# Kernel optimization log

Hardware: AMD Instinct MI355X
Metric: run time of the kernel (lower is better)

Reference implementation:

```python
import jax, jax.numpy as jnp
import numpy as np

WIN = 16
HEADS = 4


def _window_partition(x, win):
    B, H, W, C = x.shape
    x = x.reshape(B, H // win, win, W // win, win, C)
    x = x.transpose(0, 1, 3, 2, 4, 5)
    return x.reshape(-1, win * win, C)


def _reverse_window_partition(x, win, H, W):
    N, _, C = x.shape
    x = x.reshape(-1, H // win, W // win, win, win, C)
    x = x.transpose(0, 1, 3, 2, 4, 5)
    return x.reshape(-1, H, W, C)


def setup_inputs() -> dict:
    key = jax.random.key(0)
    ks = jax.random.split(key, 7)
    B, H, W, C = 2, 256, 256, 96
    s = 0.02
    return {
        "x": jax.random.normal(ks[0], (B, H, W, C), jnp.float32),
        "qkv_w": jax.random.normal(ks[1], (C, 3 * C), jnp.float32) * s,
        "qkv_b": jax.random.normal(ks[2], (3 * C,), jnp.float32) * s,
        "pe_w": jax.random.normal(ks[3], (3, 3, 1, C), jnp.float32) * s,  # depthwise HWIO
        "pe_b": jax.random.normal(ks[4], (C,), jnp.float32) * s,
        "out_w": jax.random.normal(ks[5], (C, C), jnp.float32) * s,
        "out_b": jax.random.normal(ks[6], (C,), jnp.float32) * s,
    }


def reference(x, qkv_w, qkv_b, pe_w, pe_b, out_w, out_b):
    B, H, W, C = x.shape
    win, heads = WIN, HEADS
    hd = C // heads

    z = _window_partition(x, win)
    N, S, _ = z.shape

    qkv = z @ qkv_w + qkv_b                       # (N, S, 3C)
    # headify then chunk(3): each head's 3*hd channels split into q,k,v
    qkv = qkv.reshape(N, S, heads, 3, hd).transpose(0, 2, 3, 1, 4)  # (N, h, 3, S, hd)
    q, k, v = qkv[:, :, 0], qkv[:, :, 1], qkv[:, :, 2]

    # Locally-enhanced PE: depthwise 3x3 conv on de-headified v
    v_img = v.transpose(0, 2, 1, 3).reshape(N, win, win, C)  # NHWC
    lepe = jax.lax.conv_general_dilated(
        v_img, pe_w, (1, 1), 'SAME',
        dimension_numbers=('NHWC', 'HWIO', 'NHWC'),
        feature_group_count=C) + pe_b
    lepe = lepe.reshape(N, S, heads, hd).transpose(0, 2, 1, 3)  # (N, h, S, hd)

    # per-window SDPA (default scale 1/sqrt(hd))
    scale = 1.0 / jnp.sqrt(jnp.asarray(hd, x.dtype))
    attn = jax.nn.softmax(jnp.einsum('nhsd,nhtd->nhst', q, k) * scale, axis=-1)
    o = jnp.einsum('nhst,nhtd->nhsd', attn, v) + lepe

    o = o.transpose(0, 2, 1, 3).reshape(N, S, C)
    o = _reverse_window_partition(o, win, H, W)   # (B, H, W, C)
    return o @ out_w + out_b
```

## Files before the change

### kernel.cpp

```cpp
#include <hip/hip_runtime.h>


typedef __attribute__((ext_vector_type(8))) short bf16x8;
typedef __attribute__((ext_vector_type(4))) float f32x4;

#define MFMA(a, b, c) __builtin_amdgcn_mfma_f32_16x16x32_bf16(a, b, c, 0, 0, 0)

#if __has_builtin(__builtin_amdgcn_exp2f)
#define EXP2F(x) __builtin_amdgcn_exp2f(x)
#else
#define EXP2F(x) exp2f(x)
#endif

#define SCALE2 (0.20412414523193154f * 1.4426950408889634f)

#define OFF_WT   0u
#define OFF_B2   55296u
#define OFF_WTO  56448u
#define OFF_Q    75008u
#define OFF_K    33629440u
#define OFF_VT   58795264u

__device__ __forceinline__ unsigned short f2bf(float f) {
    union { float f; unsigned int u; } v; v.f = f;
    unsigned int u = v.u;
    unsigned int r = (u + 0x7FFFu + ((u >> 16) & 1u)) >> 16;
    return (unsigned short)r;
}
__device__ __forceinline__ float bf2f(unsigned short h) {
    union { unsigned int u; float f; } v; v.u = ((unsigned int)h) << 16;
    return v.f;
}

__global__ void prep_kernel(const float* __restrict__ qkv_w,
                            const float* __restrict__ qkv_b,
                            const float* __restrict__ out_w,
                            unsigned short* __restrict__ wt,
                            float* __restrict__ b2,
                            unsigned short* __restrict__ wto) {
    const int stride = gridDim.x * 256;
    int i0 = blockIdx.x * 256 + threadIdx.x;
    for (int i = i0; i < 288 * 96; i += stride) {
        const int c = i / 96, k = i % 96;
        float v = qkv_w[k * 288 + c];
        if ((c % 72) < 24) v *= SCALE2;
        wt[i] = f2bf(v);
    }
    for (int i = i0; i < 288; i += stride) {
        float v = qkv_b[i];
        if ((i % 72) < 24) v *= SCALE2;
        b2[i] = v;
    }
    for (int i = i0; i < 96 * 96; i += stride) {
        const int c = i / 96, k = i % 96;
        wto[i] = f2bf(out_w[k * 96 + c]);
    }
}

__launch_bounds__(256, 2)
__global__ void qkv_kernel(const float* __restrict__ x,
                           const unsigned short* __restrict__ wt,
                           const float* __restrict__ b2,
                           unsigned short* __restrict__ Qb,
                           unsigned short* __restrict__ Kb,
                           unsigned short* __restrict__ VTb) {
    __shared__ unsigned short z[256 * 104];
    const int n = blockIdx.x, tid = threadIdx.x;
    const int bW = n >> 8, hy = (n >> 4) & 15, wx = n & 15;

    for (int i = tid; i < 256 * 24; i += 256) {
        const int tok = i / 24, c4 = i % 24;
        const int y = tok >> 4, xx = tok & 15;
        const size_t row = (size_t)((bW * 256 + hy * 16 + y) * 256 + wx * 16 + xx);
        const float4 v = *(const float4*)(x + row * 96 + c4 * 4);
        ushort4 p; p.x = f2bf(v.x); p.y = f2bf(v.y); p.z = f2bf(v.z); p.w = f2bf(v.w);
        *(ushort4*)&z[tok * 104 + c4 * 4] = p;
    }
    for (int i = tid; i < 1024; i += 256) {
        const int h = i >> 8, tok = i & 255;
        uint4 zz = {0, 0, 0, 0};
        *(uint4*)(Qb + ((size_t)(n * 4 + h) * 256 + tok) * 32 + 24) = zz;
    }
    __syncthreads();

    const int w = tid >> 6, l = tid & 63;
    const int lm = l & 15, lq = l >> 4;

    bf16x8 af[3][3];
#pragma unroll
    for (int mt = 0; mt < 3; mt++) {
        const int chrow = w * 72 + mt * 16 + lm;
#pragma unroll
        for (int ks = 0; ks < 3; ks++)
            af[mt][ks] = *(const bf16x8*)(wt + chrow * 96 + ks * 32 + lq * 8);
    }
    for (int nt = 0; nt < 16; nt++) {
        bf16x8 bz[3];
#pragma unroll
        for (int ks = 0; ks < 3; ks++)
            bz[ks] = *(const bf16x8*)&z[(nt * 16 + lm) * 104 + ks * 32 + lq * 8];
#pragma unroll
        for (int mt = 0; mt < 3; mt++) {
            f32x4 acc = {0.f, 0.f, 0.f, 0.f};
#pragma unroll
            for (int ks = 0; ks < 3; ks++) acc = MFMA(af[mt][ks], bz[ks], acc);
            const int r48 = mt * 16 + lq * 4;
            const float4 bias = *(const float4*)(b2 + w * 72 + r48);
            const int kind = r48 / 24;
            const int idx = r48 % 24;
            const int tok = nt * 16 + lm;
            ushort4 pk;
            pk.x = f2bf(acc[0] + bias.x); pk.y = f2bf(acc[1] + bias.y);
            pk.z = f2bf(acc[2] + bias.z); pk.w = f2bf(acc[3] + bias.w);
            unsigned short* dst = kind
                ? (Kb + ((size_t)(n * 4 + w) * 256 + tok) * 24 + idx)
                : (Qb + ((size_t)(n * 4 + w) * 256 + tok) * 32 + idx);
            *(ushort4*)dst = pk;
        }
    }

    for (int tt = 0; tt < 4; tt++) {
        const int gtt = w * 4 + tt;
        bf16x8 az[3];
#pragma unroll
        for (int ks = 0; ks < 3; ks++)
            az[ks] = *(const bf16x8*)&z[(gtt * 16 + lm) * 104 + ks * 32 + lq * 8];
#pragma unroll
        for (int nv = 0; nv < 6; nv++) {
            const int j = nv * 16 + lm;
            const int vrow = (j / 24) * 72 + 48 + (j % 24);
            f32x4 acc = {0.f, 0.f, 0.f, 0.f};
#pragma unroll
            for (int ks = 0; ks < 3; ks++) {
                const bf16x8 bw = *(const bf16x8*)(wt + vrow * 96 + ks * 32 + lq * 8);
                acc = MFMA(az[ks], bw, acc);
            }
            const float bv = b2[vrow];
            const int tokb = gtt * 16 + lq * 4;
            ushort4 pk;
            pk.x = f2bf(acc[0] + bv); pk.y = f2bf(acc[1] + bv);
            pk.z = f2bf(acc[2] + bv); pk.w = f2bf(acc[3] + bv);
            *(ushort4*)(VTb + ((size_t)(n * 4 + (j / 24)) * 24 + (j % 24)) * 256 + tokb) = pk;
        }
    }
}

__launch_bounds__(256, 2)
__global__ void attn_kernel(const unsigned short* Qb,
                            const unsigned short* __restrict__ Kb,
                            const unsigned short* __restrict__ VTb,
                            const float* __restrict__ pe_w,
                            const float* __restrict__ pe_b,
                            unsigned short* Ob) {
    __shared__ unsigned short sVT[32 * 264];
    __shared__ unsigned short sP[4 * 64 * 40];
    __shared__ float sPW[9 * 24];
    __shared__ float sPB[24];

    const int n = blockIdx.x, h = blockIdx.y, tid = threadIdx.x;
    const int nh = n * 4 + h;
    const int w = tid >> 6, l = tid & 63;
    const int lm = l & 15, lq = l >> 4;

    for (int i = tid; i < 24 * 64; i += 256) {
        const int row = i >> 6, c = i & 63;
        *(ushort4*)&sVT[row * 264 + c * 4] =
            *(const ushort4*)(VTb + ((size_t)nh * 24 + row) * 256 + c * 4);
    }
    for (int i = tid; i < 8 * 64; i += 256) {
        const int row = 24 + (i >> 6), c = i & 63;
        const unsigned short fill = (row == 24) ? (unsigned short)0x3F80 : (unsigned short)0;
        ushort4 p; p.x = fill; p.y = fill; p.z = fill; p.w = fill;
        *(ushort4*)&sVT[row * 264 + c * 4] = p;
    }
    for (int i = tid; i < 216; i += 256) sPW[i] = pe_w[(i / 24) * 96 + h * 24 + (i % 24)];
    if (tid < 24) sPB[tid] = pe_b[h * 24 + tid];

    const int qbase = w * 64;
    bf16x8 qf[4];
#pragma unroll
    for (int b = 0; b < 4; b++)
        qf[b] = *(const bf16x8*)(Qb + ((size_t)nh * 256 + qbase + b * 16 + lm) * 32 + lq * 8);
    __syncthreads();

    f32x4 oa[4][2];
#pragma unroll
    for (int b = 0; b < 4; b++)
#pragma unroll
        for (int c = 0; c < 2; c++) oa[b][c] = (f32x4){0.f, 0.f, 0.f, 0.f};

    unsigned short* Pw = &sP[w * 64 * 40];

    for (int kc = 0; kc < 8; kc++) {
#pragma unroll
        for (int a = 0; a < 2; a++) {
            const int key = kc * 32 + a * 16 + lm;
            const bf16x8 kf =
                *(const bf16x8*)(Kb + ((size_t)nh * 256 + key) * 24 + lq * 8);
            f32x4 s[4];
#pragma unroll
            for (int b = 0; b < 4; b++)
                s[b] = MFMA(kf, qf[b], ((f32x4){0.f, 0.f, 0.f, 0.f}));
#pragma unroll
            for (int b = 0; b < 4; b++) {
                ushort4 pk;
                pk.x = f2bf(EXP2F(s[b][0])); pk.y = f2bf(EXP2F(s[b][1]));
                pk.z = f2bf(EXP2F(s[b][2])); pk.w = f2bf(EXP2F(s[b][3]));
                *(ushort4*)&Pw[(b * 16 + lm) * 40 + a * 16 + lq * 4] = pk;
            }
        }
        bf16x8 pa[4], vb[2];
#pragma unroll
        for (int b = 0; b < 4; b++)
            pa[b] = *(const bf16x8*)&Pw[(b * 16 + lm) * 40 + lq * 8];
#pragma unroll
        for (int c = 0; c < 2; c++)
            vb[c] = *(const bf16x8*)&sVT[(c * 16 + lm) * 264 + kc * 32 + lq * 8];
#pragma unroll
        for (int b = 0; b < 4; b++)
#pragma unroll
            for (int c = 0; c < 2; c++) oa[b][c] = MFMA(pa[b], vb[c], oa[b][c]);
    }

#pragma unroll
    for (int b = 0; b < 4; b++) {
        float rinv[4];
#pragma unroll
        for (int r = 0; r < 4; r++) {
            const float ls = __shfl(oa[b][1][r], (l & 48) | 8, 64);
            rinv[r] = 1.0f / ls;
        }
#pragma unroll
        for (int c = 0; c < 2; c++) {
            const int ch = c * 16 + lm;
            if (ch < 24) {
#pragma unroll
                for (int r = 0; r < 4; r++) {
                    const int t = qbase + b * 16 + lq * 4 + r;
                    const int y = t >> 4, xx = t & 15;
                    float lep = sPB[ch];
#pragma unroll
                    for (int ta = 0; ta < 9; ta++) {
                        const int ny = y + ta / 3 - 1, nx = xx + ta % 3 - 1;
                        if ((unsigned)ny < 16u && (unsigned)nx < 16u)
                            lep += bf2f(sVT[ch * 264 + ny * 16 + nx]) * sPW[ta * 24 + ch];
                    }
                    const float val = oa[b][c][r] * rinv[r] + lep;
                    Ob[(size_t)nh * 8192 + t * 24 + ch] = f2bf(val);
                }
            }
        }
    }
}

__launch_bounds__(256, 2)
__global__ void outproj_kernel(const unsigned short* __restrict__ Ob,
                               const unsigned short* __restrict__ wto,
                               const float* __restrict__ out_b,
                               float* __restrict__ out) {
    const int n = blockIdx.x, tid = threadIdx.x;
    const int w = tid >> 6, l = tid & 63;
    const int lm = l & 15, lq = l >> 4;
    const int bW = n >> 8, hy = (n >> 4) & 15, wx = n & 15;

    bf16x8 af[4][3];
#pragma unroll
    for (int tt = 0; tt < 4; tt++) {
        const int tok = w * 64 + tt * 16 + lm;
#pragma unroll
        for (int ks = 0; ks < 3; ks++) {
            const int kb = ks * 32 + lq * 8;
            const int hh = kb / 24, j = kb % 24;
            af[tt][ks] = *(const bf16x8*)(Ob + ((size_t)(n * 4 + hh)) * 8192 + tok * 24 + j);
        }
    }
#pragma unroll
    for (int nt = 0; nt < 6; nt++) {
        bf16x8 bw[3];
#pragma unroll
        for (int ks = 0; ks < 3; ks++)
            bw[ks] = *(const bf16x8*)(wto + (nt * 16 + lm) * 96 + ks * 32 + lq * 8);
        const float bias = out_b[nt * 16 + lm];
#pragma unroll
        for (int tt = 0; tt < 4; tt++) {
            f32x4 acc = {0.f, 0.f, 0.f, 0.f};
#pragma unroll
            for (int ks = 0; ks < 3; ks++) acc = MFMA(af[tt][ks], bw[ks], acc);
            const int tokb = w * 64 + tt * 16 + lq * 4;
#pragma unroll
            for (int r = 0; r < 4; r++) {
                const int t = tokb + r;
                const size_t grow =
                    (size_t)((bW * 256 + hy * 16 + (t >> 4)) * 256 + wx * 16 + (t & 15));
                out[grow * 96 + nt * 16 + lm] = acc[r] + bias;
            }
        }
    }
}

extern "C" void kernel_launch(void* const* d_in, const int* in_sizes, int n_in,
                              void* d_out, int out_size, void* d_ws, size_t ws_size,
                              hipStream_t stream) {
    const float* x     = (const float*)d_in[0];
    const float* qkv_w = (const float*)d_in[1];
    const float* qkv_b = (const float*)d_in[2];
    const float* pe_w  = (const float*)d_in[3];
    const float* pe_b  = (const float*)d_in[4];
    const float* out_w = (const float*)d_in[5];
    const float* out_b = (const float*)d_in[6];
    float* out = (float*)d_out;

    char* ws = (char*)d_ws;
    unsigned short* wt  = (unsigned short*)(ws + OFF_WT);
    float*          b2  = (float*)(ws + OFF_B2);
    unsigned short* wto = (unsigned short*)(ws + OFF_WTO);
    unsigned short* Qb  = (unsigned short*)(ws + OFF_Q);
    unsigned short* Kb  = (unsigned short*)(ws + OFF_K);
    unsigned short* VTb = (unsigned short*)(ws + OFF_VT);

    prep_kernel<<<72, 256, 0, stream>>>(qkv_w, qkv_b, out_w, wt, b2, wto);
    qkv_kernel<<<512, 256, 0, stream>>>(x, wt, b2, Qb, Kb, VTb);
    attn_kernel<<<dim3(512, 4), 256, 0, stream>>>(Qb, Kb, VTb, pe_w, pe_b, Qb );
    outproj_kernel<<<512, 256, 0, stream>>>(Qb, wto, out_b, out);
}
```

Baseline: 218.2 us.

## Fuse attention with output projection and split QKV projection across half-windows

Merges the attention and output-projection kernels into one kernel per window that loops over the four heads. Each head's normalized output goes through LDS and is multiplied into the out-projection accumulators in registers, so the Ob round trip through global memory and one launch are gone. The QKV kernel now handles half a window per block (1024 blocks, occupancy hint 4), stores Q unpadded at stride 24 (zeroing the pad lanes in registers instead), and uses packed bf16 conversion. Other changes: K fragments are prefetched one chunk ahead, a register-blocked LEPE stencil, and a fast reciprocal. The cost is lower grid parallelism in the fused kernel (512 blocks instead of 2048) and more register pressure from 24 accumulator tiles.

```diff
diff --git a/kernel.cpp b/kernel.cpp
--- a/kernel.cpp
+++ b/kernel.cpp
@@ -17,19 +17,34 @@
 #define OFF_WT   0u
 #define OFF_B2   55296u
 #define OFF_WTO  56448u
-#define OFF_Q    75008u
-#define OFF_K    33629440u
-#define OFF_VT   58795264u
+#define OFF_Q    75904u
+#define OFF_K    25241728u
+#define OFF_VT   50407552u
 
 __device__ __forceinline__ unsigned short f2bf(float f) {
     union { float f; unsigned int u; } v; v.f = f;
     unsigned int u = v.u;
-    unsigned int r = (u + 0x7FFFu + ((u >> 16) & 1u)) >> 16;
-    return (unsigned short)r;
+    return (unsigned short)((u + 0x7FFFu + ((u >> 16) & 1u)) >> 16);
 }
 __device__ __forceinline__ float bf2f(unsigned short h) {
     union { unsigned int u; float f; } v; v.u = ((unsigned int)h) << 16;
     return v.f;
+}
+__device__ __forceinline__ unsigned int pk2bf(float a, float b) {
+#if __has_builtin(__builtin_amdgcn_cvt_pk_bf16_f32)
+    auto p = __builtin_amdgcn_cvt_pk_bf16_f32(a, b);
+    union { decltype(p) v; unsigned int u; } cv; cv.v = p;
+    return cv.u;
+#else
+    return (unsigned int)f2bf(a) | ((unsigned int)f2bf(b) << 16);
+#endif
+}
+__device__ __forceinline__ float frcp(float x) {
+#if __has_builtin(__builtin_amdgcn_rcpf)
+    return __builtin_amdgcn_rcpf(x);
+#else
+    return 1.0f / x;
+#endif
 }
 
 __global__ void prep_kernel(const float* __restrict__ qkv_w,
@@ -57,29 +72,28 @@
     }
 }
 
-__launch_bounds__(256, 2)
+__launch_bounds__(256, 4)
 __global__ void qkv_kernel(const float* __restrict__ x,
                            const unsigned short* __restrict__ wt,
                            const float* __restrict__ b2,
                            unsigned short* __restrict__ Qb,
                            unsigned short* __restrict__ Kb,
                            unsigned short* __restrict__ VTb) {
-    __shared__ unsigned short z[256 * 104];
-    const int n = blockIdx.x, tid = threadIdx.x;
+    __shared__ unsigned short z[128 * 104];
+    const int blk = blockIdx.x;
+    const int n = blk >> 1, half = blk & 1;
+    const int T0 = half << 7;
+    const int tid = threadIdx.x;
     const int bW = n >> 8, hy = (n >> 4) & 15, wx = n & 15;
 
-    for (int i = tid; i < 256 * 24; i += 256) {
-        const int tok = i / 24, c4 = i % 24;
+    for (int i = tid; i < 128 * 24; i += 256) {
+        const int tl = i / 24, c4 = i % 24;
+        const int tok = T0 + tl;
         const int y = tok >> 4, xx = tok & 15;
         const size_t row = (size_t)((bW * 256 + hy * 16 + y) * 256 + wx * 16 + xx);
         const float4 v = *(const float4*)(x + row * 96 + c4 * 4);
-        ushort4 p; p.x = f2bf(v.x); p.y = f2bf(v.y); p.z = f2bf(v.z); p.w = f2bf(v.w);
-        *(ushort4*)&z[tok * 104 + c4 * 4] = p;
-    }
-    for (int i = tid; i < 1024; i += 256) {
-        const int h = i >> 8, tok = i & 255;
-        uint4 zz = {0, 0, 0, 0};
-        *(uint4*)(Qb + ((size_t)(n * 4 + h) * 256 + tok) * 32 + 24) = zz;
+        uint2 pk; pk.x = pk2bf(v.x, v.y); pk.y = pk2bf(v.z, v.w);
+        *(uint2*)&z[tl * 104 + c4 * 4] = pk;
     }
     __syncthreads();
 
@@ -88,13 +102,12 @@
 
     bf16x8 af[3][3];
 #pragma unroll
-    for (int mt = 0; mt < 3; mt++) {
-        const int chrow = w * 72 + mt * 16 + lm;
+    for (int mt = 0; mt < 3; mt++)
 #pragma unroll
         for (int ks = 0; ks < 3; ks++)
-            af[mt][ks] = *(const bf16x8*)(wt + chrow * 96 + ks * 32 + lq * 8);
-    }
-    for (int nt = 0; nt < 16; nt++) {
+            af[mt][ks] = *(const bf16x8*)(wt + (w * 72 + mt * 16 + lm) * 96 + ks * 32 + lq * 8);
+
+    for (int nt = 0; nt < 8; nt++) {
         bf16x8 bz[3];
 #pragma unroll
         for (int ks = 0; ks < 3; ks++)
@@ -106,21 +119,19 @@
             for (int ks = 0; ks < 3; ks++) acc = MFMA(af[mt][ks], bz[ks], acc);
             const int r48 = mt * 16 + lq * 4;
             const float4 bias = *(const float4*)(b2 + w * 72 + r48);
-            const int kind = r48 / 24;
-            const int idx = r48 % 24;
-            const int tok = nt * 16 + lm;
-            ushort4 pk;
-            pk.x = f2bf(acc[0] + bias.x); pk.y = f2bf(acc[1] + bias.y);
-            pk.z = f2bf(acc[2] + bias.z); pk.w = f2bf(acc[3] + bias.w);
-            unsigned short* dst = kind
-                ? (Kb + ((size_t)(n * 4 + w) * 256 + tok) * 24 + idx)
-                : (Qb + ((size_t)(n * 4 + w) * 256 + tok) * 32 + idx);
-            *(ushort4*)dst = pk;
-        }
-    }
-
-    for (int tt = 0; tt < 4; tt++) {
-        const int gtt = w * 4 + tt;
+            const int kind = r48 / 24, idx = r48 % 24;
+            const int tok = T0 + nt * 16 + lm;
+            uint2 pk;
+            pk.x = pk2bf(acc[0] + bias.x, acc[1] + bias.y);
+            pk.y = pk2bf(acc[2] + bias.z, acc[3] + bias.w);
+            unsigned short* dst = kind ? Kb : Qb;
+            *(uint2*)(dst + ((size_t)(n * 4 + w) * 256 + tok) * 24 + idx) = pk;
+        }
+    }
+
+#pragma unroll
+    for (int tt2 = 0; tt2 < 2; tt2++) {
+        const int gtt = w * 2 + tt2;
         bf16x8 az[3];
 #pragma unroll
         for (int ks = 0; ks < 3; ks++)
@@ -136,163 +147,188 @@
                 acc = MFMA(az[ks], bw, acc);
             }
             const float bv = b2[vrow];
-            const int tokb = gtt * 16 + lq * 4;
-            ushort4 pk;
-            pk.x = f2bf(acc[0] + bv); pk.y = f2bf(acc[1] + bv);
-            pk.z = f2bf(acc[2] + bv); pk.w = f2bf(acc[3] + bv);
-            *(ushort4*)(VTb + ((size_t)(n * 4 + (j / 24)) * 24 + (j % 24)) * 256 + tokb) = pk;
+            const int tokb = T0 + gtt * 16 + lq * 4;
+            uint2 pk;
+            pk.x = pk2bf(acc[0] + bv, acc[1] + bv);
+            pk.y = pk2bf(acc[2] + bv, acc[3] + bv);
+            *(uint2*)(VTb + ((size_t)(n * 4 + j / 24) * 24 + (j % 24)) * 256 + tokb) = pk;
         }
     }
 }
 
 __launch_bounds__(256, 2)
-__global__ void attn_kernel(const unsigned short* Qb,
-                            const unsigned short* __restrict__ Kb,
-                            const unsigned short* __restrict__ VTb,
-                            const float* __restrict__ pe_w,
-                            const float* __restrict__ pe_b,
-                            unsigned short* Ob) {
+__global__ void attn_out_kernel(const unsigned short* __restrict__ Qb,
+                                const unsigned short* __restrict__ Kb,
+                                const unsigned short* __restrict__ VTb,
+                                const float* __restrict__ pe_w,
+                                const float* __restrict__ pe_b,
+                                const unsigned short* __restrict__ wto,
+                                const float* __restrict__ out_b,
+                                float* __restrict__ out) {
     __shared__ unsigned short sVT[32 * 264];
-    __shared__ unsigned short sP[4 * 64 * 40];
-    __shared__ float sPW[9 * 24];
+    __shared__ unsigned short sPO[4 * 64 * 40];
+    __shared__ float sPW[216];
     __shared__ float sPB[24];
 
-    const int n = blockIdx.x, h = blockIdx.y, tid = threadIdx.x;
-    const int nh = n * 4 + h;
+    const int n = blockIdx.x, tid = threadIdx.x;
     const int w = tid >> 6, l = tid & 63;
     const int lm = l & 15, lq = l >> 4;
-
-    for (int i = tid; i < 24 * 64; i += 256) {
-        const int row = i >> 6, c = i & 63;
-        *(ushort4*)&sVT[row * 264 + c * 4] =
-            *(const ushort4*)(VTb + ((size_t)nh * 24 + row) * 256 + c * 4);
-    }
-    for (int i = tid; i < 8 * 64; i += 256) {
-        const int row = 24 + (i >> 6), c = i & 63;
-        const unsigned short fill = (row == 24) ? (unsigned short)0x3F80 : (unsigned short)0;
-        ushort4 p; p.x = fill; p.y = fill; p.z = fill; p.w = fill;
-        *(ushort4*)&sVT[row * 264 + c * 4] = p;
-    }
-    for (int i = tid; i < 216; i += 256) sPW[i] = pe_w[(i / 24) * 96 + h * 24 + (i % 24)];
-    if (tid < 24) sPB[tid] = pe_b[h * 24 + tid];
-
     const int qbase = w * 64;
-    bf16x8 qf[4];
+    unsigned short* Pw = &sPO[w * 64 * 40];
+
+    f32x4 oacc[4][6];
 #pragma unroll
     for (int b = 0; b < 4; b++)
-        qf[b] = *(const bf16x8*)(Qb + ((size_t)nh * 256 + qbase + b * 16 + lm) * 32 + lq * 8);
-    __syncthreads();
-
-    f32x4 oa[4][2];
-#pragma unroll
-    for (int b = 0; b < 4; b++)
-#pragma unroll
-        for (int c = 0; c < 2; c++) oa[b][c] = (f32x4){0.f, 0.f, 0.f, 0.f};
-
-    unsigned short* Pw = &sP[w * 64 * 40];
-
-    for (int kc = 0; kc < 8; kc++) {
-#pragma unroll
-        for (int a = 0; a < 2; a++) {
-            const int key = kc * 32 + a * 16 + lm;
-            const bf16x8 kf =
-                *(const bf16x8*)(Kb + ((size_t)nh * 256 + key) * 24 + lq * 8);
-            f32x4 s[4];
-#pragma unroll
-            for (int b = 0; b < 4; b++)
-                s[b] = MFMA(kf, qf[b], ((f32x4){0.f, 0.f, 0.f, 0.f}));
+#pragma unroll
+        for (int nt = 0; nt < 6; nt++) oacc[b][nt] = (f32x4){0.f, 0.f, 0.f, 0.f};
+
+    for (int h = 0; h < 4; h++) {
+        const size_t nh = (size_t)(n * 4 + h);
+        __syncthreads();
+        for (int i = tid; i < 24 * 64; i += 256) {
+            const int row = i >> 6, c = i & 63;
+            *(ushort4*)&sVT[row * 264 + c * 4] =
+                *(const ushort4*)(VTb + (nh * 24 + row) * 256 + c * 4);
+        }
+        if (tid < 64) {
+            ushort4 ones; ones.x = ones.y = ones.z = ones.w = (unsigned short)0x3F80;
+            *(ushort4*)&sVT[24 * 264 + tid * 4] = ones;
+        }
+        for (int i = tid; i < 216; i += 256) sPW[i] = pe_w[(i / 24) * 96 + h * 24 + (i % 24)];
+        if (tid < 24) sPB[tid] = pe_b[h * 24 + tid];
+
+        bf16x8 qf[4];
+#pragma unroll
+        for (int b = 0; b < 4; b++) {
+            bf16x8 qv = *(const bf16x8*)(Qb + (nh * 256 + qbase + b * 16 + lm) * 24 + lq * 8);
+            if (lq == 3) qv = (bf16x8)(short)0;
+            qf[b] = qv;
+        }
+        __syncthreads();
+
+        f32x4 oa[4][2];
+#pragma unroll
+        for (int b = 0; b < 4; b++)
+#pragma unroll
+            for (int c = 0; c < 2; c++) oa[b][c] = (f32x4){0.f, 0.f, 0.f, 0.f};
+
+        bf16x8 kfn[2];
+#pragma unroll
+        for (int a = 0; a < 2; a++)
+            kfn[a] = *(const bf16x8*)(Kb + (nh * 256 + a * 16 + lm) * 24 + lq * 8);
+
+        for (int kc = 0; kc < 8; kc++) {
+            bf16x8 kfc[2] = {kfn[0], kfn[1]};
+            if (kc < 7) {
+#pragma unroll
+                for (int a = 0; a < 2; a++)
+                    kfn[a] = *(const bf16x8*)(Kb + (nh * 256 + (kc + 1) * 32 + a * 16 + lm) * 24 + lq * 8);
+            }
+#pragma unroll
+            for (int a = 0; a < 2; a++) {
+                f32x4 s[4];
+#pragma unroll
+                for (int b = 0; b < 4; b++)
+                    s[b] = MFMA(kfc[a], qf[b], ((f32x4){0.f, 0.f, 0.f, 0.f}));
+#pragma unroll
+                for (int b = 0; b < 4; b++) {
+                    uint2 pk;
+                    pk.x = pk2bf(EXP2F(s[b][0]), EXP2F(s[b][1]));
+                    pk.y = pk2bf(EXP2F(s[b][2]), EXP2F(s[b][3]));
+                    *(uint2*)&Pw[(b * 16 + lm) * 40 + a * 16 + lq * 4] = pk;
+                }
+            }
+            bf16x8 vb[2];
+#pragma unroll
+            for (int c = 0; c < 2; c++)
+                vb[c] = *(const bf16x8*)&sVT[(c * 16 + lm) * 264 + kc * 32 + lq * 8];
 #pragma unroll
             for (int b = 0; b < 4; b++) {
-                ushort4 pk;
-                pk.x = f2bf(EXP2F(s[b][0])); pk.y = f2bf(EXP2F(s[b][1]));
-                pk.z = f2bf(EXP2F(s[b][2])); pk.w = f2bf(EXP2F(s[b][3]));
-                *(ushort4*)&Pw[(b * 16 + lm) * 40 + a * 16 + lq * 4] = pk;
-            }
-        }
-        bf16x8 pa[4], vb[2];
-#pragma unroll
-        for (int b = 0; b < 4; b++)
-            pa[b] = *(const bf16x8*)&Pw[(b * 16 + lm) * 40 + lq * 8];
-#pragma unroll
-        for (int c = 0; c < 2; c++)
-            vb[c] = *(const bf16x8*)&sVT[(c * 16 + lm) * 264 + kc * 32 + lq * 8];
-#pragma unroll
-        for (int b = 0; b < 4; b++)
-#pragma unroll
-            for (int c = 0; c < 2; c++) oa[b][c] = MFMA(pa[b], vb[c], oa[b][c]);
-    }
-
-#pragma unroll
-    for (int b = 0; b < 4; b++) {
-        float rinv[4];
-#pragma unroll
-        for (int r = 0; r < 4; r++) {
-            const float ls = __shfl(oa[b][1][r], (l & 48) | 8, 64);
-            rinv[r] = 1.0f / ls;
-        }
+                const bf16x8 pa = *(const bf16x8*)&Pw[(b * 16 + lm) * 40 + lq * 8];
+#pragma unroll
+                for (int c = 0; c < 2; c++) oa[b][c] = MFMA(pa, vb[c], oa[b][c]);
+            }
+        }
+
+        {
+            uint4 zz = {0u, 0u, 0u, 0u};
+            *(uint4*)&Pw[l * 40 + 24] = zz;
+        }
+        float w9[2][9], pb2[2];
 #pragma unroll
         for (int c = 0; c < 2; c++) {
             const int ch = c * 16 + lm;
             if (ch < 24) {
 #pragma unroll
-                for (int r = 0; r < 4; r++) {
-                    const int t = qbase + b * 16 + lq * 4 + r;
-                    const int y = t >> 4, xx = t & 15;
-                    float lep = sPB[ch];
-#pragma unroll
-                    for (int ta = 0; ta < 9; ta++) {
-                        const int ny = y + ta / 3 - 1, nx = xx + ta % 3 - 1;
-                        if ((unsigned)ny < 16u && (unsigned)nx < 16u)
-                            lep += bf2f(sVT[ch * 264 + ny * 16 + nx]) * sPW[ta * 24 + ch];
+                for (int ta = 0; ta < 9; ta++) w9[c][ta] = sPW[ta * 24 + ch];
+                pb2[c] = sPB[ch];
+            }
+        }
+#pragma unroll
+        for (int b = 0; b < 4; b++) {
+            float rinv[4];
+#pragma unroll
+            for (int r = 0; r < 4; r++)
+                rinv[r] = frcp(__shfl(oa[b][1][r], (l & 48) | 8, 64));
+            const int y = w * 4 + b;
+            const int x0 = lq * 4;
+#pragma unroll
+            for (int c = 0; c < 2; c++) {
+                const int ch = c * 16 + lm;
+                if (ch < 24) {
+                    float lep[4] = {pb2[c], pb2[c], pb2[c], pb2[c]};
+                    const unsigned short* vbase = &sVT[ch * 264];
+#pragma unroll
+                    for (int dy = -1; dy <= 1; dy++) {
+                        const int ny = y + dy;
+                        if ((unsigned)ny > 15u) continue;
+                        const unsigned short* vrow = vbase + ny * 16;
+                        const float wl = w9[c][(dy + 1) * 3 + 0];
+                        const float wm = w9[c][(dy + 1) * 3 + 1];
+                        const float wr = w9[c][(dy + 1) * 3 + 2];
+#pragma unroll
+                        for (int d = -1; d <= 4; d++) {
+                            const int xx = x0 + d;
+                            if ((unsigned)xx > 15u) continue;
+                            const float v = bf2f(vrow[xx]);
+                            if (d - 1 >= 0 && d - 1 <= 3) lep[d - 1] = fmaf(v, wr, lep[d - 1]);
+                            if (d >= 0 && d <= 3)         lep[d]     = fmaf(v, wm, lep[d]);
+                            if (d + 1 <= 3)               lep[d + 1] = fmaf(v, wl, lep[d + 1]);
+                        }
                     }
-                    const float val = oa[b][c][r] * rinv[r] + lep;
-                    Ob[(size_t)nh * 8192 + t * 24 + ch] = f2bf(val);
+#pragma unroll
+                    for (int r = 0; r < 4; r++) {
+                        const float val = oa[b][c][r] * rinv[r] + lep[r];
+                        Pw[(b * 16 + lq * 4 + r) * 40 + ch] = f2bf(val);
+                    }
                 }
             }
         }
-    }
-}
-
-__launch_bounds__(256, 2)
-__global__ void outproj_kernel(const unsigned short* __restrict__ Ob,
-                               const unsigned short* __restrict__ wto,
-                               const float* __restrict__ out_b,
-                               float* __restrict__ out) {
-    const int n = blockIdx.x, tid = threadIdx.x;
-    const int w = tid >> 6, l = tid & 63;
-    const int lm = l & 15, lq = l >> 4;
+
+        bf16x8 aO[4];
+#pragma unroll
+        for (int b = 0; b < 4; b++)
+            aO[b] = *(const bf16x8*)&Pw[(b * 16 + lm) * 40 + lq * 8];
+#pragma unroll
+        for (int nt = 0; nt < 6; nt++) {
+            const bf16x8 bwf = *(const bf16x8*)(wto + (nt * 16 + lm) * 96 + h * 24 + lq * 8);
+#pragma unroll
+            for (int b = 0; b < 4; b++) oacc[b][nt] = MFMA(aO[b], bwf, oacc[b][nt]);
+        }
+    }
+
     const int bW = n >> 8, hy = (n >> 4) & 15, wx = n & 15;
-
-    bf16x8 af[4][3];
-#pragma unroll
-    for (int tt = 0; tt < 4; tt++) {
-        const int tok = w * 64 + tt * 16 + lm;
-#pragma unroll
-        for (int ks = 0; ks < 3; ks++) {
-            const int kb = ks * 32 + lq * 8;
-            const int hh = kb / 24, j = kb % 24;
-            af[tt][ks] = *(const bf16x8*)(Ob + ((size_t)(n * 4 + hh)) * 8192 + tok * 24 + j);
-        }
-    }
 #pragma unroll
     for (int nt = 0; nt < 6; nt++) {
-        bf16x8 bw[3];
-#pragma unroll
-        for (int ks = 0; ks < 3; ks++)
-            bw[ks] = *(const bf16x8*)(wto + (nt * 16 + lm) * 96 + ks * 32 + lq * 8);
         const float bias = out_b[nt * 16 + lm];
 #pragma unroll
-        for (int tt = 0; tt < 4; tt++) {
-            f32x4 acc = {0.f, 0.f, 0.f, 0.f};
-#pragma unroll
-            for (int ks = 0; ks < 3; ks++) acc = MFMA(af[tt][ks], bw[ks], acc);
-            const int tokb = w * 64 + tt * 16 + lq * 4;
+        for (int b = 0; b < 4; b++) {
 #pragma unroll
             for (int r = 0; r < 4; r++) {
-                const int t = tokb + r;
+                const int t = qbase + b * 16 + lq * 4 + r;
                 const size_t grow =
                     (size_t)((bW * 256 + hy * 16 + (t >> 4)) * 256 + wx * 16 + (t & 15));
-                out[grow * 96 + nt * 16 + lm] = acc[r] + bias;
+                out[grow * 96 + nt * 16 + lm] = oacc[b][nt][r] + bias;
             }
         }
     }
@@ -319,7 +355,6 @@
     unsigned short* VTb = (unsigned short*)(ws + OFF_VT);
 
     prep_kernel<<<72, 256, 0, stream>>>(qkv_w, qkv_b, out_w, wt, b2, wto);
-    qkv_kernel<<<512, 256, 0, stream>>>(x, wt, b2, Qb, Kb, VTb);
-    attn_kernel<<<dim3(512, 4), 256, 0, stream>>>(Qb, Kb, VTb, pe_w, pe_b, Qb );
-    outproj_kernel<<<512, 256, 0, stream>>>(Qb, wto, out_b, out);
-}
+    qkv_kernel<<<1024, 256, 0, stream>>>(x, wt, b2, Qb, Kb, VTb);
+    attn_out_kernel<<<512, 256, 0, stream>>>(Qb, Kb, VTb, pe_w, pe_b, wto, out_b, out);
+}
```

Result: faster. 200.0 us (-8.3%).
